# Kernel tuning notes

Hardware: AMD Instinct MI355X
Metric: run time of the kernel (lower is better)

## Reference

```python
import jax, jax.numpy as jnp
import numpy as np

HEADS = 8
DIM_HEAD = 64
SCALE = DIM_HEAD ** -0.5


def setup_inputs() -> dict:
    key = jax.random.key(0)
    ks = jax.random.split(key, 6)
    b, n, d = 2, 4096, 1024
    inner = HEADS * DIM_HEAD  # 512
    x = jax.random.normal(ks[0], (b, n, d), dtype=jnp.float32)
    Wq = jax.random.normal(ks[1], (d, inner), dtype=jnp.float32) * (d ** -0.5)
    Wk = jax.random.normal(ks[2], (d, inner), dtype=jnp.float32) * (d ** -0.5)
    Wv = jax.random.normal(ks[3], (d, inner), dtype=jnp.float32) * (d ** -0.5)
    Wout = jax.random.normal(ks[4], (inner, d), dtype=jnp.float32) * (inner ** -0.5)
    bout = jnp.zeros((d,), dtype=jnp.float32)
    return {"x": x, "Wq": Wq, "Wk": Wk, "Wv": Wv, "Wout": Wout, "bout": bout}


def reference(x, Wq, Wk, Wv, Wout, bout):
    b, n, _ = x.shape
    h, dh = HEADS, DIM_HEAD
    # self-attention: context = x
    q = (x @ Wq).reshape(b, n, h, dh).transpose(0, 2, 1, 3)  # b h n d
    k = (x @ Wk).reshape(b, n, h, dh).transpose(0, 2, 1, 3)
    v = (x @ Wv).reshape(b, n, h, dh).transpose(0, 2, 1, 3)
    sim = jnp.einsum('bhid,bhjd->bhij', q, k) * SCALE  # full score matrix
    attn = jax.nn.softmax(sim, axis=-1)
    out = jnp.einsum('bhij,bhjd->bhid', attn, v)
    out = out.transpose(0, 2, 1, 3).reshape(b, n, h * dh)  # b n (h d)
    return out @ Wout + bout
```

## Files before the change

### kernel.cpp

```cpp
#include <hip/hip_runtime.h>
#include <hip/hip_bf16.h>

typedef __bf16 bf16x8 __attribute__((ext_vector_type(8)));
typedef __bf16 bf16x4 __attribute__((ext_vector_type(4)));
typedef float floatx4 __attribute__((ext_vector_type(4)));

#define MFMA16(a, b, c) __builtin_amdgcn_mfma_f32_16x16x32_bf16((a), (b), (c), 0, 0, 0)

__device__ __forceinline__ void stage16(const __bf16* g, __bf16* lds_base) {
  __builtin_amdgcn_global_load_lds(
      (__attribute__((address_space(1))) void*)(void*)g,
      (__attribute__((address_space(3))) void*)lds_base, 16, 0, 0);
}

__global__ void detect_dtype(const unsigned int* __restrict__ x, int* __restrict__ flag) {
  __shared__ int cnt;
  if (threadIdx.x == 0) cnt = 0;
  __syncthreads();
  int c = 0;
  for (int i = threadIdx.x; i < 4096; i += 256) {
    const unsigned f = (x[i] >> 7) & 0xFF;
    c += (f >= 100 && f <= 140) ? 1 : 0;
  }
  atomicAdd(&cnt, c);
  __syncthreads();
  if (threadIdx.x == 0) *flag = (cnt > 2048) ? 1 : 0;
}

__global__ __launch_bounds__(256) void convert_x(const void* __restrict__ src,
                                                 __bf16* __restrict__ dst,
                                                 const int* __restrict__ flagp) {
  const int isbf = *flagp;
  const size_t i = ((size_t)blockIdx.x * 256 + threadIdx.x) * 8;
  if (isbf) {
    *(bf16x8*)(dst + i) = *(const bf16x8*)((const __bf16*)src + i);
  } else {
    const float4 f0 = *(const float4*)((const float*)src + i);
    const float4 f1 = *(const float4*)((const float*)src + i + 4);
    bf16x8 v;
    v[0] = (__bf16)f0.x; v[1] = (__bf16)f0.y; v[2] = (__bf16)f0.z; v[3] = (__bf16)f0.w;
    v[4] = (__bf16)f1.x; v[5] = (__bf16)f1.y; v[6] = (__bf16)f1.z; v[7] = (__bf16)f1.w;
    *(bf16x8*)(dst + i) = v;
  }
}

__global__ __launch_bounds__(256) void transpose3_conv(
    const void* __restrict__ s0, const void* __restrict__ s1,
    const void* __restrict__ s2, __bf16* __restrict__ dst,
    int R, int C, const int* __restrict__ flagp) {
  __shared__ __bf16 t[32][33];
  const int isbf = *flagp;
  const void* src = (blockIdx.z == 0) ? s0 : (blockIdx.z == 1) ? s1 : s2;
  __bf16* d = dst + (size_t)blockIdx.z * R * C;
  const int bx = blockIdx.x * 32, by = blockIdx.y * 32;
  const int x = threadIdx.x & 31, y0 = threadIdx.x >> 5;
#pragma unroll
  for (int i = y0; i < 32; i += 8) {
    const size_t idx = (size_t)(by + i) * C + bx + x;
    t[i][x] = isbf ? ((const __bf16*)src)[idx] : (__bf16)(((const float*)src)[idx]);
  }
  __syncthreads();
#pragma unroll
  for (int i = y0; i < 32; i += 8) d[(size_t)(bx + i) * R + by + x] = t[x][i];
}

__global__ __launch_bounds__(256) void transpose_conv(const void* __restrict__ src,
                                                      __bf16* __restrict__ dst,
                                                      int R, int C,
                                                      const int* __restrict__ flagp) {
  __shared__ __bf16 t[32][33];
  const int isbf = *flagp;
  const int bx = blockIdx.x * 32, by = blockIdx.y * 32;
  const int x = threadIdx.x & 31, y0 = threadIdx.x >> 5;
#pragma unroll
  for (int i = y0; i < 32; i += 8) {
    const size_t idx = (size_t)(by + i) * C + bx + x;
    t[i][x] = isbf ? ((const __bf16*)src)[idx] : (__bf16)(((const float*)src)[idx]);
  }
  __syncthreads();
#pragma unroll
  for (int i = y0; i < 32; i += 8) dst[(size_t)(bx + i) * R + by + x] = t[x][i];
}

__global__ __launch_bounds__(256) void vp_transpose(const __bf16* __restrict__ V,
                                                    __bf16* __restrict__ VP) {
  alignas(16) __shared__ __bf16 t[64][64];
  const int bh = blockIdx.y, s0 = blockIdx.x * 64;
  const int row = threadIdx.x >> 2, part = threadIdx.x & 3;
  const __bf16* src = V + (size_t)bh * 262144 + (size_t)(s0 + row) * 64 + part * 16;
  *(bf16x8*)&t[row][part * 16] = *(const bf16x8*)src;
  *(bf16x8*)&t[row][part * 16 + 8] = *(const bf16x8*)(src + 8);
  __syncthreads();
  const int d = row, og = part;
  bf16x8 w0, w1;
#pragma unroll
  for (int e = 0; e < 8; e++) {
    const int o0 = og * 16 + e, o1 = og * 16 + 8 + e;
    w0[e] = t[(o0 & 3) * 16 + (o0 >> 2)][d];
    w1[e] = t[(o1 & 3) * 16 + (o1 >> 2)][d];
  }
  __bf16* dst = VP + (size_t)bh * 262144 + (size_t)d * 4096 + s0 + og * 16;
  *(bf16x8*)dst = w0;
  *(bf16x8*)(dst + 8) = w1;
}

__global__ __launch_bounds__(256) void gemm_bt(
    const __bf16* __restrict__ A, const __bf16* __restrict__ Bt,
    void* __restrict__ Cv, void* __restrict__ Cv2, int M, int N, int K,
    const void* __restrict__ bias, int permute, int egress_dual,
    size_t zsC, const int* __restrict__ flagp) {
  alignas(16) __shared__ __bf16 As[2][128 * 32];
  alignas(16) __shared__ __bf16 Bs[2][128 * 32];
  const int isbf = *flagp;
  const int gx = gridDim.x;
  const int nwg = gx * gridDim.y;
  const int orig = blockIdx.x + blockIdx.y * gx;
  const int qq = nwg >> 3;
  const int swz = (orig & 7) * qq + (orig >> 3);
  const int bx = swz % gx, by = swz / gx;

  const int tid = threadIdx.x;
  const int wave = tid >> 6, lane = tid & 63;
  const int m0 = by * 128, n0 = bx * 128;
  const int wm = (wave & 1) * 64, wn = (wave >> 1) * 64;
  const int fr = lane & 15, fq = lane >> 4;

  const floatx4 zero4 = {0.f, 0.f, 0.f, 0.f};
  floatx4 acc[4][4];
#pragma unroll
  for (int i = 0; i < 4; i++)
#pragma unroll
    for (int j = 0; j < 4; j++) acc[i][j] = zero4;

  const int lrow = lane >> 2;
  const int lk = (lane & 3) * 8;
  const int NT = K >> 5;

#pragma unroll
  for (int cc = 0; cc < 2; ++cc) {
    const int c = 2 * wave + cc;
    stage16(A + (size_t)(m0 + c * 16 + lrow) * K + lk, &As[0][c * 512]);
    stage16(Bt + (size_t)(n0 + c * 16 + lrow) * K + lk, &Bs[0][c * 512]);
  }

  for (int t = 0; t < NT; ++t) {
    const int cur = t & 1;
    if (t + 1 < NT) {
      const int k1 = (t + 1) << 5;
#pragma unroll
      for (int cc = 0; cc < 2; ++cc) {
        const int c = 2 * wave + cc;
        stage16(A + (size_t)(m0 + c * 16 + lrow) * K + k1 + lk, &As[1 - cur][c * 512]);
        stage16(Bt + (size_t)(n0 + c * 16 + lrow) * K + k1 + lk, &Bs[1 - cur][c * 512]);
      }
      asm volatile("s_waitcnt vmcnt(4)" ::: "memory");
    } else {
      asm volatile("s_waitcnt vmcnt(0)" ::: "memory");
    }
    __builtin_amdgcn_s_barrier();
    __builtin_amdgcn_sched_barrier(0);
    bf16x8 af[4], bg[4];
#pragma unroll
    for (int mt = 0; mt < 4; mt++)
      af[mt] = *(const bf16x8*)&As[cur][(wm + mt * 16 + fr) * 32 + fq * 8];
#pragma unroll
    for (int nt = 0; nt < 4; nt++)
      bg[nt] = *(const bf16x8*)&Bs[cur][(wn + nt * 16 + fr) * 32 + fq * 8];
#pragma unroll
    for (int mt = 0; mt < 4; mt++)
#pragma unroll
      for (int nt = 0; nt < 4; nt++)
        acc[mt][nt] = MFMA16(af[mt], bg[nt], acc[mt][nt]);
    __builtin_amdgcn_sched_barrier(0);
    __builtin_amdgcn_s_barrier();
  }

  const float qs = (permute && n0 < 512) ? 0.18033688011112042f
                                         : 1.0f;
#pragma unroll
  for (int mt = 0; mt < 4; mt++)
#pragma unroll
    for (int nt = 0; nt < 4; nt++)
#pragma unroll
      for (int r = 0; r < 4; r++) {
        const int row = m0 + wm + mt * 16 + fq * 4 + r;
        const int col = n0 + wn + nt * 16 + fr;
        float v = acc[mt][nt][r] * qs;
        if (bias)
          v += isbf ? (float)((const __bf16*)bias)[col] : ((const float*)bias)[col];
        if (permute) {
          const int plane = col >> 9;
          const int pc = col & 511;
          const int bh = ((row >> 12) << 3) + (pc >> 6);
          const int s = row & 4095, d = col & 63;
          const size_t pidx = (size_t)bh * 262144 + (size_t)s * 64 + d;
          if (plane == 2)
            ((__bf16*)Cv2)[pidx] = (__bf16)v;
          else
            ((__bf16*)Cv)[(size_t)plane * zsC + pidx] = (__bf16)v;
        } else {
          const size_t idx = (size_t)row * N + col;
          if (egress_dual && !isbf)
            ((float*)Cv)[idx] = v;
          else
            ((__bf16*)Cv)[idx] = (__bf16)v;
        }
      }
}

#define ATT_S 4096
__global__ __launch_bounds__(256, 2) void attn_flash(
    const __bf16* __restrict__ Qa, const __bf16* __restrict__ Ka,
    const __bf16* __restrict__ VPa, __bf16* __restrict__ O) {
  alignas(16) __shared__ __bf16 Kl[3][64 * 64];
  alignas(16) __shared__ __bf16 Vl[3][64 * 64];
  alignas(16) __shared__ __bf16 Pl[4 * 32 * 64];
  const int tid = threadIdx.x, wave = tid >> 6, lane = tid & 63;
  const int orig = blockIdx.x + blockIdx.y * 32;
  const int swz = (orig & 7) * 64 + (orig >> 3);
  const int qx = swz & 31, bh = swz >> 5;
  const int b = bh >> 3, h = bh & 7;
  const int q0 = qx * 128 + wave * 32;
  const int fr = lane & 15, fq = lane >> 4;
  const __bf16* Qb = Qa + (size_t)bh * ATT_S * 64;
  const __bf16* Kb = Ka + (size_t)bh * ATT_S * 64;
  const __bf16* Vb = VPa + (size_t)bh * ATT_S * 64;

  const int sw0 = ((fq ^ (fr & 7)) * 8);
  const int sw1 = (((fq + 4) ^ (fr & 7)) * 8);
  const int r0 = tid >> 3;
  const int ssw = (((tid & 7) ^ (r0 & 7)) * 8);

  bf16x8 aq[2][2];
#pragma unroll
  for (int mt = 0; mt < 2; mt++)
#pragma unroll
    for (int kt = 0; kt < 2; kt++)
      aq[mt][kt] = *(const bf16x8*)(Qb + (size_t)(q0 + mt * 16 + fr) * 64 + kt * 32 + fq * 8);

  const floatx4 zero4 = {0.f, 0.f, 0.f, 0.f};
  floatx4 o[2][4];
  float lsum[2][4];
#pragma unroll
  for (int mt = 0; mt < 2; mt++) {
#pragma unroll
    for (int nt = 0; nt < 4; nt++) o[mt][nt] = zero4;
#pragma unroll
    for (int r = 0; r < 4; r++) lsum[mt][r] = 0.f;
  }

  const int JT = ATT_S / 64;

#pragma unroll
  for (int t0 = 0; t0 < 2; ++t0) {
    const int kv = t0 * 64;
    stage16(Kb + (size_t)(kv + r0) * 64 + ssw, &Kl[t0][wave * 512]);
    stage16(Kb + (size_t)(kv + 32 + r0) * 64 + ssw, &Kl[t0][2048 + wave * 512]);
    stage16(Vb + (size_t)r0 * 4096 + kv + ssw, &Vl[t0][wave * 512]);
    stage16(Vb + (size_t)(32 + r0) * 4096 + kv + ssw, &Vl[t0][2048 + wave * 512]);
  }

  for (int j = 0; j < JT; ++j) {
    const int cur = j % 3;
    if (j + 2 < JT) {
      const int sl = (j + 2) % 3;
      const int kv2 = (j + 2) * 64;
      stage16(Kb + (size_t)(kv2 + r0) * 64 + ssw, &Kl[sl][wave * 512]);
      stage16(Kb + (size_t)(kv2 + 32 + r0) * 64 + ssw, &Kl[sl][2048 + wave * 512]);
      stage16(Vb + (size_t)r0 * 4096 + kv2 + ssw, &Vl[sl][wave * 512]);
      stage16(Vb + (size_t)(32 + r0) * 4096 + kv2 + ssw, &Vl[sl][2048 + wave * 512]);
      asm volatile("s_waitcnt vmcnt(8)" ::: "memory");
    } else if (j + 1 < JT) {
      asm volatile("s_waitcnt vmcnt(4)" ::: "memory");
    } else {
      asm volatile("s_waitcnt vmcnt(0)" ::: "memory");
    }
    __builtin_amdgcn_s_barrier();
    __builtin_amdgcn_sched_barrier(0);
    const __bf16* Klc = Kl[cur];
    const __bf16* Vlc = Vl[cur];

    floatx4 s4[2][4];
    __builtin_amdgcn_s_setprio(1);
#pragma unroll
    for (int nt = 0; nt < 4; nt++) {
      bf16x8 bk0 = *(const bf16x8*)&Klc[(nt * 16 + fr) * 64 + sw0];
      bf16x8 bk1 = *(const bf16x8*)&Klc[(nt * 16 + fr) * 64 + sw1];
#pragma unroll
      for (int mt = 0; mt < 2; mt++) {
        floatx4 zz = zero4;
        zz = MFMA16(aq[mt][0], bk0, zz);
        zz = MFMA16(aq[mt][1], bk1, zz);
        s4[mt][nt] = zz;
      }
    }
    __builtin_amdgcn_s_setprio(0);

#pragma unroll
    for (int mt = 0; mt < 2; mt++)
#pragma unroll
      for (int r = 0; r < 4; r++) {
        bf16x4 pv;
        float psum = 0.f;
#pragma unroll
        for (int nt = 0; nt < 4; nt++) {
          const float p = __builtin_amdgcn_exp2f(s4[mt][nt][r]);
          pv[nt] = (__bf16)p;
          psum += p;
        }
        lsum[mt][r] += psum;
        const int row = wave * 32 + mt * 16 + fq * 4 + r;
        const int vg = (fr >> 1) ^ ((fq * 4 + r) & 7);
        *(bf16x4*)&Pl[row * 64 + vg * 8 + (fr & 1) * 4] = pv;
      }
    asm volatile("s_waitcnt lgkmcnt(0)" ::: "memory");

    bf16x8 bv[4][2];
#pragma unroll
    for (int nt = 0; nt < 4; nt++) {
      bv[nt][0] = *(const bf16x8*)&Vlc[(nt * 16 + fr) * 64 + sw0];
      bv[nt][1] = *(const bf16x8*)&Vlc[(nt * 16 + fr) * 64 + sw1];
    }
    __builtin_amdgcn_s_setprio(1);
#pragma unroll
    for (int mt = 0; mt < 2; mt++) {
      const int prow = (wave * 32 + mt * 16 + fr) * 64;
      bf16x8 ap0 = *(const bf16x8*)&Pl[prow + sw0];
      bf16x8 ap1 = *(const bf16x8*)&Pl[prow + sw1];
#pragma unroll
      for (int nt = 0; nt < 4; nt++) {
        o[mt][nt] = MFMA16(ap0, bv[nt][0], o[mt][nt]);
        o[mt][nt] = MFMA16(ap1, bv[nt][1], o[mt][nt]);
      }
    }
    __builtin_amdgcn_s_setprio(0);
    __builtin_amdgcn_sched_barrier(0);
    __builtin_amdgcn_s_barrier();
  }

#pragma unroll
  for (int off = 1; off < 16; off <<= 1)
#pragma unroll
    for (int mt = 0; mt < 2; mt++)
#pragma unroll
      for (int r = 0; r < 4; r++) lsum[mt][r] += __shfl_xor(lsum[mt][r], off, 64);

#pragma unroll
  for (int mt = 0; mt < 2; mt++)
#pragma unroll
    for (int r = 0; r < 4; r++) {
      const float inv = 1.0f / lsum[mt][r];
      const int row = q0 + mt * 16 + fq * 4 + r;
      __bf16* Orow = O + (size_t)(b * ATT_S + row) * 512 + h * 64;
#pragma unroll
      for (int nt = 0; nt < 4; nt++)
        Orow[nt * 16 + fr] = (__bf16)(o[mt][nt][r] * inv);
    }
}

extern "C" void kernel_launch(void* const* d_in, const int* in_sizes, int n_in,
                              void* d_out, int out_size, void* d_ws, size_t ws_size,
                              hipStream_t stream) {
  (void)in_sizes; (void)n_in; (void)out_size; (void)ws_size;
  const void* x = d_in[0];
  const void* Wq = d_in[1];
  const void* Wk = d_in[2];
  const void* Wv = d_in[3];
  const void* Wout = d_in[4];
  const void* bout = d_in[5];

  char* ws = (char*)d_ws;
  int* flag = (int*)ws;
  __bf16* wtq = (__bf16*)(ws + (1u << 20));
  __bf16* wto = (__bf16*)(ws + (4u << 20));
  __bf16* Q = (__bf16*)(ws + (5u << 20));
  __bf16* K = (__bf16*)(ws + (13u << 20));
  __bf16* VP = (__bf16*)(ws + (21u << 20));
  __bf16* O = (__bf16*)(ws + (29u << 20));
  __bf16* Vtmp = O;
  __bf16* xbf = (__bf16*)(ws + (38u << 20));

  detect_dtype<<<1, 256, 0, stream>>>((const unsigned int*)x, flag);

  transpose3_conv<<<dim3(16, 32, 3), 256, 0, stream>>>(Wq, Wk, Wv, wtq, 1024, 512, flag);
  transpose_conv<<<dim3(32, 16), 256, 0, stream>>>(Wout, wto, 512, 1024, flag);

  convert_x<<<4096, 256, 0, stream>>>(x, xbf, flag);

  gemm_bt<<<dim3(12, 64, 1), 256, 0, stream>>>(
      xbf, wtq, Q, Vtmp, 8192, 1536, 1024, nullptr, 1, 0,
      (size_t)8192 * 512, flag);

  vp_transpose<<<dim3(64, 16), 256, 0, stream>>>(Vtmp, VP);

  attn_flash<<<dim3(ATT_S / 128, 16), 256, 0, stream>>>(Q, K, VP, O);

  gemm_bt<<<dim3(8, 64, 1), 256, 0, stream>>>(
      O, wto, d_out, nullptr, 8192, 1024, 512, bout, 0, 1, 0, flag);
}
```

Before: 254.0 us.

## Fuse V transpose into QKV GEMM epilogue via LDS-staged coalesced stores

The QKV projection GEMM now stages its output tile in shared memory (the staging buffers are merged into one larger array) and writes Q/K rows with 16-byte vector stores. The V plane is written directly in the permuted transposed layout the attention kernel expects. This removes the separate vp_transpose kernel and its extra pass over V, and replaces scattered scalar epilogue stores with coalesced ones. The cost is a larger LDS footprint per block (about 34KB) plus an extra barrier in the epilogue.

```diff
diff --git a/kernel.cpp b/kernel.cpp
--- a/kernel.cpp
+++ b/kernel.cpp
@@ -82,35 +82,12 @@
   for (int i = y0; i < 32; i += 8) dst[(size_t)(bx + i) * R + by + x] = t[x][i];
 }
 
-__global__ __launch_bounds__(256) void vp_transpose(const __bf16* __restrict__ V,
-                                                    __bf16* __restrict__ VP) {
-  alignas(16) __shared__ __bf16 t[64][64];
-  const int bh = blockIdx.y, s0 = blockIdx.x * 64;
-  const int row = threadIdx.x >> 2, part = threadIdx.x & 3;
-  const __bf16* src = V + (size_t)bh * 262144 + (size_t)(s0 + row) * 64 + part * 16;
-  *(bf16x8*)&t[row][part * 16] = *(const bf16x8*)src;
-  *(bf16x8*)&t[row][part * 16 + 8] = *(const bf16x8*)(src + 8);
-  __syncthreads();
-  const int d = row, og = part;
-  bf16x8 w0, w1;
-#pragma unroll
-  for (int e = 0; e < 8; e++) {
-    const int o0 = og * 16 + e, o1 = og * 16 + 8 + e;
-    w0[e] = t[(o0 & 3) * 16 + (o0 >> 2)][d];
-    w1[e] = t[(o1 & 3) * 16 + (o1 >> 2)][d];
-  }
-  __bf16* dst = VP + (size_t)bh * 262144 + (size_t)d * 4096 + s0 + og * 16;
-  *(bf16x8*)dst = w0;
-  *(bf16x8*)(dst + 8) = w1;
-}
-
 __global__ __launch_bounds__(256) void gemm_bt(
     const __bf16* __restrict__ A, const __bf16* __restrict__ Bt,
     void* __restrict__ Cv, void* __restrict__ Cv2, int M, int N, int K,
     const void* __restrict__ bias, int permute, int egress_dual,
     size_t zsC, const int* __restrict__ flagp) {
-  alignas(16) __shared__ __bf16 As[2][128 * 32];
-  alignas(16) __shared__ __bf16 Bs[2][128 * 32];
+  __shared__ __attribute__((aligned(16))) __bf16 SH[17408];
   const int isbf = *flagp;
   const int gx = gridDim.x;
   const int nwg = gx * gridDim.y;
@@ -139,8 +116,8 @@
 #pragma unroll
   for (int cc = 0; cc < 2; ++cc) {
     const int c = 2 * wave + cc;
-    stage16(A + (size_t)(m0 + c * 16 + lrow) * K + lk, &As[0][c * 512]);
-    stage16(Bt + (size_t)(n0 + c * 16 + lrow) * K + lk, &Bs[0][c * 512]);
+    stage16(A + (size_t)(m0 + c * 16 + lrow) * K + lk, &SH[c * 512]);
+    stage16(Bt + (size_t)(n0 + c * 16 + lrow) * K + lk, &SH[8192 + c * 512]);
   }
 
   for (int t = 0; t < NT; ++t) {
@@ -150,8 +127,10 @@
 #pragma unroll
       for (int cc = 0; cc < 2; ++cc) {
         const int c = 2 * wave + cc;
-        stage16(A + (size_t)(m0 + c * 16 + lrow) * K + k1 + lk, &As[1 - cur][c * 512]);
-        stage16(Bt + (size_t)(n0 + c * 16 + lrow) * K + k1 + lk, &Bs[1 - cur][c * 512]);
+        stage16(A + (size_t)(m0 + c * 16 + lrow) * K + k1 + lk,
+                &SH[(1 - cur) * 4096 + c * 512]);
+        stage16(Bt + (size_t)(n0 + c * 16 + lrow) * K + k1 + lk,
+                &SH[8192 + (1 - cur) * 4096 + c * 512]);
       }
       asm volatile("s_waitcnt vmcnt(4)" ::: "memory");
     } else {
@@ -162,10 +141,10 @@
     bf16x8 af[4], bg[4];
 #pragma unroll
     for (int mt = 0; mt < 4; mt++)
-      af[mt] = *(const bf16x8*)&As[cur][(wm + mt * 16 + fr) * 32 + fq * 8];
+      af[mt] = *(const bf16x8*)&SH[cur * 4096 + (wm + mt * 16 + fr) * 32 + fq * 8];
 #pragma unroll
     for (int nt = 0; nt < 4; nt++)
-      bg[nt] = *(const bf16x8*)&Bs[cur][(wn + nt * 16 + fr) * 32 + fq * 8];
+      bg[nt] = *(const bf16x8*)&SH[8192 + cur * 4096 + (wn + nt * 16 + fr) * 32 + fq * 8];
 #pragma unroll
     for (int mt = 0; mt < 4; mt++)
 #pragma unroll
@@ -175,37 +154,70 @@
     __builtin_amdgcn_s_barrier();
   }
 
-  const float qs = (permute && n0 < 512) ? 0.18033688011112042f
-                                         : 1.0f;
-#pragma unroll
-  for (int mt = 0; mt < 4; mt++)
-#pragma unroll
-    for (int nt = 0; nt < 4; nt++)
-#pragma unroll
-      for (int r = 0; r < 4; r++) {
-        const int row = m0 + wm + mt * 16 + fq * 4 + r;
-        const int col = n0 + wn + nt * 16 + fr;
-        float v = acc[mt][nt][r] * qs;
-        if (bias)
-          v += isbf ? (float)((const __bf16*)bias)[col] : ((const float*)bias)[col];
-        if (permute) {
-          const int plane = col >> 9;
-          const int pc = col & 511;
-          const int bh = ((row >> 12) << 3) + (pc >> 6);
-          const int s = row & 4095, d = col & 63;
-          const size_t pidx = (size_t)bh * 262144 + (size_t)s * 64 + d;
-          if (plane == 2)
-            ((__bf16*)Cv2)[pidx] = (__bf16)v;
-          else
-            ((__bf16*)Cv)[(size_t)plane * zsC + pidx] = (__bf16)v;
-        } else {
+  if (permute) {
+    const float qs = (n0 < 512) ? 0.18033688011112042f : 1.0f;
+#pragma unroll
+    for (int mt = 0; mt < 4; mt++)
+#pragma unroll
+      for (int nt = 0; nt < 4; nt++)
+#pragma unroll
+        for (int r = 0; r < 4; r++) {
+          const int lr = wm + mt * 16 + fq * 4 + r;
+          const int lc = wn + nt * 16 + fr;
+          SH[lr * 136 + lc] = (__bf16)(acc[mt][nt][r] * qs);
+        }
+    __syncthreads();
+    const int bB = m0 >> 12;
+    if (n0 < 1024) {
+      const int plane = n0 >> 9;
+      const int lr = tid >> 1, ch = (tid & 1) << 6;
+      const int col0 = n0 + ch;
+      const int bh = bB * 8 + ((col0 & 511) >> 6);
+      __bf16* rowp = (__bf16*)Cv + (size_t)plane * zsC + (size_t)bh * 262144 +
+                     (size_t)((m0 + lr) & 4095) * 64;
+      const __bf16* srcp = &SH[lr * 136 + ch];
+#pragma unroll
+      for (int k = 0; k < 8; ++k)
+        *(bf16x8*)(rowp + k * 8) = *(const bf16x8*)(srcp + k * 8);
+    } else {
+      const int dloc = tid >> 1, gh = tid & 1;
+      const int col0 = n0 + dloc;
+      const int bh = bB * 8 + ((col0 & 511) >> 6);
+      const int d = col0 & 63;
+      __bf16* outp = (__bf16*)Cv2 + (size_t)bh * 262144 + (size_t)d * 4096 +
+                     ((m0 & 4095) + (gh << 6));
+      const int srow0 = gh << 6;
+#pragma unroll
+      for (int k = 0; k < 8; ++k) {
+        bf16x8 w;
+#pragma unroll
+        for (int e = 0; e < 8; ++e) {
+          const int p = k * 8 + e;
+          const int tsrc = ((p & 3) << 4) | (p >> 2);
+          w[e] = SH[(srow0 + tsrc) * 136 + dloc];
+        }
+        *(bf16x8*)(outp + k * 8) = w;
+      }
+    }
+  } else {
+#pragma unroll
+    for (int mt = 0; mt < 4; mt++)
+#pragma unroll
+      for (int nt = 0; nt < 4; nt++)
+#pragma unroll
+        for (int r = 0; r < 4; r++) {
+          const int row = m0 + wm + mt * 16 + fq * 4 + r;
+          const int col = n0 + wn + nt * 16 + fr;
+          float v = acc[mt][nt][r];
+          if (bias)
+            v += isbf ? (float)((const __bf16*)bias)[col] : ((const float*)bias)[col];
           const size_t idx = (size_t)row * N + col;
           if (egress_dual && !isbf)
             ((float*)Cv)[idx] = v;
           else
             ((__bf16*)Cv)[idx] = (__bf16)v;
         }
-      }
+  }
 }
 
 #define ATT_S 4096
@@ -377,7 +389,6 @@
   __bf16* K = (__bf16*)(ws + (13u << 20));
   __bf16* VP = (__bf16*)(ws + (21u << 20));
   __bf16* O = (__bf16*)(ws + (29u << 20));
-  __bf16* Vtmp = O;
   __bf16* xbf = (__bf16*)(ws + (38u << 20));
 
   detect_dtype<<<1, 256, 0, stream>>>((const unsigned int*)x, flag);
@@ -388,10 +399,8 @@
   convert_x<<<4096, 256, 0, stream>>>(x, xbf, flag);
 
   gemm_bt<<<dim3(12, 64, 1), 256, 0, stream>>>(
-      xbf, wtq, Q, Vtmp, 8192, 1536, 1024, nullptr, 1, 0,
+      xbf, wtq, Q, VP, 8192, 1536, 1024, nullptr, 1, 0,
       (size_t)8192 * 512, flag);
-
-  vp_transpose<<<dim3(64, 16), 256, 0, stream>>>(Vtmp, VP);
 
   attn_flash<<<dim3(ATT_S / 128, 16), 256, 0, stream>>>(Q, K, VP, O);
 
```

Result: faster. 248.5 us (-2.2%).
